# Kernel tuning notes

Measured on AMD Instinct MI355X. Metric: run time of the kernel, lower is better.

Reference implementation:

```python
import jax, jax.numpy as jnp
import numpy as np

LOG2 = float(np.log(2.0))

def shifted_softplus(x):
    return jax.nn.softplus(x) - LOG2

def setup_inputs() -> dict:
    key = jax.random.key(0)
    ks = jax.random.split(key, 12)
    N, E = 100000, 1600000
    Cin, Cout, F_, G = 128, 128, 128, 50
    x = jax.random.normal(ks[0], (N, Cin), dtype=jnp.float32)
    edge_index = jax.random.randint(ks[1], (2, E), 0, N, dtype=jnp.int64)
    edge_attr = jax.random.uniform(ks[2], (E, G), dtype=jnp.float32)
    s = lambda fan_in: 1.0 / np.sqrt(fan_in)
    lin1_w = jax.random.uniform(ks[3], (F_, Cin), jnp.float32, -s(Cin), s(Cin))
    lin1_b = jax.random.uniform(ks[4], (F_,), jnp.float32, -s(Cin), s(Cin))
    lin2_w = jax.random.uniform(ks[5], (Cout, F_), jnp.float32, -s(F_), s(F_))
    lin2_b = jax.random.uniform(ks[6], (Cout,), jnp.float32, -s(F_), s(F_))
    fn1_w = jax.random.uniform(ks[7], (F_, G), jnp.float32, -s(G), s(G))
    fn1_b = jax.random.uniform(ks[8], (F_,), jnp.float32, -s(G), s(G))
    fn2_w = jax.random.uniform(ks[9], (F_, F_), jnp.float32, -s(F_), s(F_))
    fn2_b = jax.random.uniform(ks[10], (F_,), jnp.float32, -s(F_), s(F_))
    return {"x": x, "edge_index": edge_index, "edge_attr": edge_attr,
            "lin1_w": lin1_w, "lin1_b": lin1_b, "lin2_w": lin2_w, "lin2_b": lin2_b,
            "fn1_w": fn1_w, "fn1_b": fn1_b, "fn2_w": fn2_w, "fn2_b": fn2_b}

def reference(x, edge_index, edge_attr, lin1_w, lin1_b, lin2_w, lin2_b,
              fn1_w, fn1_b, fn2_w, fn2_b):
    row, col = edge_index[0], edge_index[1]
    # filter network: [E, G] -> [E, F]
    W = shifted_softplus(edge_attr @ fn1_w.T + fn1_b) @ fn2_w.T + fn2_b
    # transform nodes then gather source features: [E, F]
    x_j = (x @ lin1_w.T + lin1_b)[col]
    msg = x_j * W
    # scatter-add over destination nodes: [N, F]
    agg = jax.ops.segment_sum(msg, row, num_segments=x.shape[0])
    return agg @ lin2_w.T + lin2_b
```

## Files before the change

### kernel.cpp

```cpp
#include <hip/hip_runtime.h>

#define NN 100000
#define NE 1600000
#define CC 128
#define GG 50
#define EPB 128
#define NSCB 98

typedef _Float16 half8 __attribute__((ext_vector_type(8)));
typedef _Float16 half2v __attribute__((ext_vector_type(2)));
typedef float f32x4 __attribute__((ext_vector_type(4)));

static __device__ __forceinline__ f32x4 mfma16(half8 a, half8 b, f32x4 c) {
    return __builtin_amdgcn_mfma_f32_16x16x32_f16(a, b, c, 0, 0, 0);
}

static __device__ __forceinline__ int perm_chan(int p) {
    return ((p >> 2) & 15) * 8 + (p >> 6) * 4 + (p & 3);
}

__global__ __launch_bounds__(256) void pack_frags(const float* fn1_w, const float* fn2_w,
                                                  _Float16* ws_frag)
{
    int tid = threadIdx.x;
    for (int s = tid; s < 1024; s += 256) {
        int l = s & 63, ks = (s >> 6) & 1, nb = s >> 7;
        int f = nb * 16 + (l & 15);
        int k0 = ks * 32 + 8 * (l >> 4);
        half8 v;
        #pragma unroll
        for (int i = 0; i < 8; i++) {
            int g = k0 + i;
            v[i] = (g < GG) ? (_Float16)fn1_w[f * GG + g] : (_Float16)0.f;
        }
        *reinterpret_cast<half8*>(&ws_frag[s * 8]) = v;
    }
    for (int s = tid; s < 2048; s += 256) {
        int l = s & 63, ks = (s >> 6) & 3, nb = s >> 8;
        int f = (l & 15) * 8 + nb;
        int k0 = ks * 32 + 8 * (l >> 4);
        const float* wp = fn2_w + f * CC + k0;
        half8 v;
        #pragma unroll
        for (int i = 0; i < 8; i++) v[i] = (_Float16)wp[i];
        *reinterpret_cast<half8*>(&ws_frag[8192 + s * 8]) = v;
    }
}

template <typename InT, typename OutT, bool DOH, bool PERMK>
__global__ __launch_bounds__(256) void lin_kernel(const InT* in, const float* w,
                                                  const float* bias, OutT* out, int nrows,
                                                  const int* hrow, int* hcnt)
{
    __shared__ __align__(16) _Float16 a_lds[64][136];
    __shared__ __align__(16) _Float16 bfrag[2048 * 8];

    int tid = threadIdx.x;
    int rowBase = blockIdx.x * 64;

    if constexpr (sizeof(InT) == 4) {
        for (int i = tid; i < 64 * 32; i += 256) {
            int r = i >> 5, c4 = i & 31;
            float4 v = {0.f, 0.f, 0.f, 0.f};
            if (rowBase + r < nrows)
                v = reinterpret_cast<const float4*>(in)[(size_t)(rowBase + r) * (CC / 4) + c4];
            a_lds[r][c4 * 4 + 0] = (_Float16)v.x;
            a_lds[r][c4 * 4 + 1] = (_Float16)v.y;
            a_lds[r][c4 * 4 + 2] = (_Float16)v.z;
            a_lds[r][c4 * 4 + 3] = (_Float16)v.w;
        }
    } else {
        for (int i = tid; i < 64 * 16; i += 256) {
            int r = i >> 4, c8 = i & 15;
            half8 v;
            #pragma unroll
            for (int k = 0; k < 8; k++) v[k] = (_Float16)0.f;
            if (rowBase + r < nrows)
                v = reinterpret_cast<const half8*>(in)[(size_t)(rowBase + r) * (CC / 8) + c8];
            *reinterpret_cast<half8*>(&a_lds[r][c8 * 8]) = v;
        }
    }
    for (int s = tid; s < 2048; s += 256) {
        int l = s & 63, ks = (s >> 6) & 3, nb = s >> 8;
        int f = nb * 16 + (l & 15);
        int k0 = ks * 32 + 8 * (l >> 4);
        const float* wrow = w + f * CC;
        half8 v;
        #pragma unroll
        for (int i = 0; i < 8; i++) {
            int k = k0 + i;
            int rk = PERMK ? perm_chan(k) : k;
            v[i] = (_Float16)wrow[rk];
        }
        *reinterpret_cast<half8*>(&bfrag[s * 8]) = v;
    }

    if constexpr (DOH) {
        int idx4 = blockIdx.x * 256 + tid;
        if (idx4 < NE / 4) {
            int4 e4 = reinterpret_cast<const int4*>(hrow)[idx4];
            atomicAdd(&hcnt[e4.x], 1);
            atomicAdd(&hcnt[e4.y], 1);
            atomicAdd(&hcnt[e4.z], 1);
            atomicAdd(&hcnt[e4.w], 1);
        }
    }
    __syncthreads();

    int wid = tid >> 6, l = tid & 63;
    int lr = l & 15, lg = l >> 4;
    int wrow = wid * 16;

    half8 afr[4];
    #pragma unroll
    for (int ks = 0; ks < 4; ks++)
        afr[ks] = *reinterpret_cast<const half8*>(&a_lds[wrow + lr][ks * 32 + 8 * lg]);

    #pragma unroll
    for (int nb = 0; nb < 8; nb++) {
        f32x4 acc = {0.f, 0.f, 0.f, 0.f};
        #pragma unroll
        for (int ks = 0; ks < 4; ks++) {
            half8 bf = *reinterpret_cast<const half8*>(&bfrag[((nb * 4 + ks) * 64 + l) * 8]);
            acc = mfma16(afr[ks], bf, acc);
        }
        float bv = bias[nb * 16 + lr];
        #pragma unroll
        for (int j = 0; j < 4; j++) {
            int r = rowBase + wrow + lg * 4 + j;
            if (r < nrows) out[(size_t)r * CC + nb * 16 + lr] = (OutT)(acc[j] + bv);
        }
    }
}

__global__ __launch_bounds__(256) void scanA(const int* cnt, int* excl, int* bsum, int n) {
    __shared__ int lds[256];
    int b = blockIdx.x, t = threadIdx.x;
    int base = b * 1024 + t * 4;
    int v[4];
    #pragma unroll
    for (int i = 0; i < 4; i++) v[i] = (base + i < n) ? cnt[base + i] : 0;
    int s = v[0] + v[1] + v[2] + v[3];
    lds[t] = s;
    __syncthreads();
    for (int off = 1; off < 256; off <<= 1) {
        int x = (t >= off) ? lds[t - off] : 0;
        __syncthreads();
        lds[t] += x;
        __syncthreads();
    }
    int incl = lds[t];
    int run = incl - s;
    #pragma unroll
    for (int i = 0; i < 4; i++) {
        if (base + i < n) excl[base + i] = run;
        run += v[i];
    }
    if (t == 255) bsum[b] = incl;
}

__global__ __launch_bounds__(128) void scanB(int* bsum, int n) {
    __shared__ int lds[128];
    int t = threadIdx.x;
    int v = (t < n) ? bsum[t] : 0;
    lds[t] = v;
    __syncthreads();
    for (int off = 1; off < 128; off <<= 1) {
        int x = (t >= off) ? lds[t - off] : 0;
        __syncthreads();
        lds[t] += x;
        __syncthreads();
    }
    if (t < n) bsum[t] = lds[t] - v;
}

__global__ __launch_bounds__(256) void scanC(int* excl, const int* bsum, int* cursor, int n) {
    int b = blockIdx.x, t = threadIdx.x;
    int off = bsum[b];
    int base = b * 1024 + t * 4;
    #pragma unroll
    for (int i = 0; i < 4; i++) {
        int idx = base + i;
        if (idx < n) {
            int val = excl[idx] + off;
            excl[idx] = val;
            cursor[idx] = val;
        }
    }
}

__global__ __launch_bounds__(512, 8) void msg_scatter_kernel(
    const _Float16* __restrict__ x1, const int* __restrict__ eidx,
    const float* __restrict__ ea, const _Float16* __restrict__ frag_ws,
    const float* __restrict__ fn1_b, const float* __restrict__ fn2_b,
    int* __restrict__ cursor, _Float16* __restrict__ msg)
{
    __shared__ __align__(16) unsigned char u_lds[EPB * CC * 2];
    __shared__ int cols_l[EPB];
    __shared__ int p_l[EPB];

    int tid = threadIdx.x;
    size_t eBase = (size_t)blockIdx.x * EPB;

    if (tid < EPB) {
        int r = eidx[eBase + tid];
        cols_l[tid] = eidx[(size_t)NE + eBase + tid];
        p_l[tid] = atomicAdd(&cursor[r], 1);
    }
    {
        const float2* eap = reinterpret_cast<const float2*>(ea + eBase * GG);
        for (int i = tid; i < EPB * 25; i += 512) {
            int e = i / 25, g2 = i - e * 25;
            float2 v = eap[i];
            int byte = e * 128 + ((g2 * 4) ^ ((e & 7) << 4));
            _Float16* p = reinterpret_cast<_Float16*>(u_lds + byte);
            p[0] = (_Float16)v.x;
            p[1] = (_Float16)v.y;
        }
        for (int i = tid; i < EPB * 14; i += 512) {
            int e = i / 14, g = (i - e * 14) + 50;
            int byte = e * 128 + ((g * 2) ^ ((e & 7) << 4));
            *reinterpret_cast<_Float16*>(u_lds + byte) = (_Float16)0.f;
        }
    }
    __syncthreads();

    int wv = tid >> 6, l = tid & 63;
    int lr = l & 15, lg = l >> 4;
    int erow = wv * 16;

    half8 a1[2];
    #pragma unroll
    for (int ks = 0; ks < 2; ks++) {
        int e = erow + lr;
        int byte = e * 128 + ((ks * 64 + lg * 16) ^ ((e & 7) << 4));
        a1[ks] = *reinterpret_cast<const half8*>(u_lds + byte);
    }
    __syncthreads();

    #pragma unroll
    for (int nb = 0; nb < 8; nb++) {
        half8 b10 = *reinterpret_cast<const half8*>(&frag_ws[((nb * 2 + 0) * 64 + l) * 8]);
        half8 b11 = *reinterpret_cast<const half8*>(&frag_ws[((nb * 2 + 1) * 64 + l) * 8]);
        f32x4 acc = {0.f, 0.f, 0.f, 0.f};
        acc = mfma16(a1[0], b10, acc);
        acc = mfma16(a1[1], b11, acc);
        float bv = fn1_b[nb * 16 + lr];
        int f = nb * 16 + lr;
        #pragma unroll
        for (int j = 0; j < 4; j++) {
            float z = acc[j] + bv;
            float t = __expf(-fabsf(z));
            float hz = fmaxf(z, 0.f) + __logf(1.f + t) - 0.69314718055994531f;
            int e = erow + lg * 4 + j;
            int byte = e * 256 + ((f * 2) ^ ((e & 7) << 4));
            *reinterpret_cast<_Float16*>(u_lds + byte) = (_Float16)hz;
        }
    }
    __syncthreads();

    half8 a2[4];
    #pragma unroll
    for (int ks = 0; ks < 4; ks++) {
        int e = erow + lr;
        int byte = e * 256 + ((ks * 64 + lg * 16) ^ ((e & 7) << 4));
        a2[ks] = *reinterpret_cast<const half8*>(u_lds + byte);
    }
    int pp[4], cc4[4];
    #pragma unroll
    for (int j = 0; j < 4; j++) {
        int e = erow + lg * 4 + j;
        pp[j] = p_l[e];
        cc4[j] = cols_l[e];
    }

    const half8* b2g = reinterpret_cast<const half8*>(frag_ws + 8192);
    #pragma unroll
    for (int hf = 0; hf < 2; hf++) {
        f32x4 acc[4];
        #pragma unroll
        for (int q = 0; q < 4; q++) {
            int nb = hf * 4 + q;
            f32x4 a = {0.f, 0.f, 0.f, 0.f};
            #pragma unroll
            for (int ks = 0; ks < 4; ks++)
                a = mfma16(a2[ks], b2g[(nb * 4 + ks) * 64 + l], a);
            acc[q] = a;
        }
        int ch0 = lr * 8 + hf * 4;
        int pos0 = hf * 64 + lr * 4;
        float4 bv = *reinterpret_cast<const float4*>(&fn2_b[ch0]);

        #pragma unroll
        for (int j = 0; j < 4; j++) {
            uint2 xp = *reinterpret_cast<const uint2*>(&x1[(size_t)cc4[j] * CC + ch0]);
            half2v x01 = __builtin_bit_cast(half2v, xp.x);
            half2v x23 = __builtin_bit_cast(half2v, xp.y);
            half2v p0, p1;
            p0[0] = (_Float16)((float)x01[0] * (acc[0][j] + bv.x));
            p0[1] = (_Float16)((float)x01[1] * (acc[1][j] + bv.y));
            p1[0] = (_Float16)((float)x23[0] * (acc[2][j] + bv.z));
            p1[1] = (_Float16)((float)x23[1] * (acc[3][j] + bv.w));
            uint2 st;
            st.x = __builtin_bit_cast(unsigned, p0);
            st.y = __builtin_bit_cast(unsigned, p1);
            *reinterpret_cast<uint2*>(&msg[(size_t)pp[j] * CC + pos0]) = st;
        }
    }
}

__global__ __launch_bounds__(512, 8) void gather_reduce_kernel(
    const _Float16* __restrict__ msg, const int* __restrict__ rowptr,
    _Float16* __restrict__ aggH)
{
    int tid = threadIdx.x;
    int r = blockIdx.x * 8 + (tid >> 6);
    int l = tid & 63;
    int e0 = rowptr[r];
    int e1 = (r == NN - 1) ? NE : rowptr[r + 1];

    const unsigned* base = reinterpret_cast<const unsigned*>(msg) + l;
    float a0 = 0.f, a1 = 0.f;
    int i = e0;
    for (; i + 1 < e1; i += 2) {
        unsigned v0 = base[(size_t)i * 64];
        unsigned v1 = base[(size_t)(i + 1) * 64];
        half2v h0 = __builtin_bit_cast(half2v, v0);
        half2v h1 = __builtin_bit_cast(half2v, v1);
        a0 += (float)h0[0] + (float)h1[0];
        a1 += (float)h0[1] + (float)h1[1];
    }
    if (i < e1) {
        half2v h = __builtin_bit_cast(half2v, base[(size_t)i * 64]);
        a0 += (float)h[0];
        a1 += (float)h[1];
    }
    half2v o;
    o[0] = (_Float16)a0;
    o[1] = (_Float16)a1;
    reinterpret_cast<unsigned*>(aggH)[(size_t)r * 64 + l] = __builtin_bit_cast(unsigned, o);
}

__global__ __launch_bounds__(512, 8) void edge_kernel_atomic(
    const _Float16* __restrict__ x1, const int* __restrict__ eidx,
    const float* __restrict__ ea, const _Float16* __restrict__ frag_ws,
    const float* __restrict__ fn1_b, const float* __restrict__ fn2_b,
    float* __restrict__ agg)
{
    __shared__ __align__(16) unsigned char u_lds[EPB * CC * 2];
    __shared__ int rows_l[EPB];
    __shared__ int cols_l[EPB];

    int tid = threadIdx.x;
    size_t eBase = (size_t)blockIdx.x * EPB;

    if (tid < EPB) {
        rows_l[tid] = eidx[eBase + tid];
        cols_l[tid] = eidx[(size_t)NE + eBase + tid];
    }
    {
        const float2* eap = reinterpret_cast<const float2*>(ea + eBase * GG);
        for (int i = tid; i < EPB * 25; i += 512) {
            int e = i / 25, g2 = i - e * 25;
            float2 v = eap[i];
            int byte = e * 128 + ((g2 * 4) ^ ((e & 7) << 4));
            _Float16* p = reinterpret_cast<_Float16*>(u_lds + byte);
            p[0] = (_Float16)v.x;
            p[1] = (_Float16)v.y;
        }
        for (int i = tid; i < EPB * 14; i += 512) {
            int e = i / 14, g = (i - e * 14) + 50;
            int byte = e * 128 + ((g * 2) ^ ((e & 7) << 4));
            *reinterpret_cast<_Float16*>(u_lds + byte) = (_Float16)0.f;
        }
    }
    __syncthreads();

    int wv = tid >> 6, l = tid & 63;
    int lr = l & 15, lg = l >> 4;
    int erow = wv * 16;

    half8 a1[2];
    #pragma unroll
    for (int ks = 0; ks < 2; ks++) {
        int e = erow + lr;
        int byte = e * 128 + ((ks * 64 + lg * 16) ^ ((e & 7) << 4));
        a1[ks] = *reinterpret_cast<const half8*>(u_lds + byte);
    }
    __syncthreads();

    #pragma unroll
    for (int nb = 0; nb < 8; nb++) {
        half8 b10 = *reinterpret_cast<const half8*>(&frag_ws[((nb * 2 + 0) * 64 + l) * 8]);
        half8 b11 = *reinterpret_cast<const half8*>(&frag_ws[((nb * 2 + 1) * 64 + l) * 8]);
        f32x4 acc = {0.f, 0.f, 0.f, 0.f};
        acc = mfma16(a1[0], b10, acc);
        acc = mfma16(a1[1], b11, acc);
        float bv = fn1_b[nb * 16 + lr];
        int f = nb * 16 + lr;
        #pragma unroll
        for (int j = 0; j < 4; j++) {
            float z = acc[j] + bv;
            float t = __expf(-fabsf(z));
            float hz = fmaxf(z, 0.f) + __logf(1.f + t) - 0.69314718055994531f;
            int e = erow + lg * 4 + j;
            int byte = e * 256 + ((f * 2) ^ ((e & 7) << 4));
            *reinterpret_cast<_Float16*>(u_lds + byte) = (_Float16)hz;
        }
    }
    __syncthreads();

    half8 a2[4];
    #pragma unroll
    for (int ks = 0; ks < 4; ks++) {
        int e = erow + lr;
        int byte = e * 256 + ((ks * 64 + lg * 16) ^ ((e & 7) << 4));
        a2[ks] = *reinterpret_cast<const half8*>(u_lds + byte);
    }
    int rr[4], cc4[4];
    #pragma unroll
    for (int j = 0; j < 4; j++) {
        int e = erow + lg * 4 + j;
        rr[j] = rows_l[e];
        cc4[j] = cols_l[e];
    }
    const half8* b2g = reinterpret_cast<const half8*>(frag_ws + 8192);
    #pragma unroll
    for (int hf = 0; hf < 2; hf++) {
        f32x4 acc[4];
        #pragma unroll
        for (int q = 0; q < 4; q++) {
            int nb = hf * 4 + q;
            f32x4 a = {0.f, 0.f, 0.f, 0.f};
            #pragma unroll
            for (int ks = 0; ks < 4; ks++)
                a = mfma16(a2[ks], b2g[(nb * 4 + ks) * 64 + l], a);
            acc[q] = a;
        }
        int ch0 = lr * 8 + hf * 4;
        float4 bv = *reinterpret_cast<const float4*>(&fn2_b[ch0]);
        #pragma unroll
        for (int j = 0; j < 4; j++) {
            uint2 xp = *reinterpret_cast<const uint2*>(&x1[(size_t)cc4[j] * CC + ch0]);
            half2v x01 = __builtin_bit_cast(half2v, xp.x);
            half2v x23 = __builtin_bit_cast(half2v, xp.y);
            float* dst = &agg[(size_t)rr[j] * CC + ch0];
            atomicAdd(dst + 0, (float)x01[0] * (acc[0][j] + bv.x));
            atomicAdd(dst + 1, (float)x01[1] * (acc[1][j] + bv.y));
            atomicAdd(dst + 2, (float)x23[0] * (acc[2][j] + bv.z));
            atomicAdd(dst + 3, (float)x23[1] * (acc[3][j] + bv.w));
        }
    }
}

extern "C" void kernel_launch(void* const* d_in, const int* in_sizes, int n_in,
                              void* d_out, int out_size, void* d_ws, size_t ws_size,
                              hipStream_t stream) {
    const float* x      = (const float*)d_in[0];
    const int*   eidx   = (const int*)d_in[1];
    const float* ea     = (const float*)d_in[2];
    const float* lin1_w = (const float*)d_in[3];
    const float* lin1_b = (const float*)d_in[4];
    const float* lin2_w = (const float*)d_in[5];
    const float* lin2_b = (const float*)d_in[6];
    const float* fn1_w  = (const float*)d_in[7];
    const float* fn1_b  = (const float*)d_in[8];
    const float* fn2_w  = (const float*)d_in[9];
    const float* fn2_b  = (const float*)d_in[10];

    float* out = (float*)d_out;

    const size_t o_frag = 0;
    const size_t o_x1h  = 65536;
    const size_t o_msg  = o_x1h + (size_t)NN * CC * 2;
    const size_t o_aggH = o_msg + (size_t)NE * CC * 2;
    const size_t o_cnt  = o_aggH + (size_t)NN * CC * 2;
    const size_t o_rp   = o_cnt + (size_t)NN * 4;
    const size_t o_cur  = o_rp + (size_t)NN * 4;
    const size_t o_bsum = o_cur + (size_t)NN * 4;
    const size_t req    = o_bsum + 512;

    _Float16* frag_ws = (_Float16*)((char*)d_ws + o_frag);
    _Float16* x1h     = (_Float16*)((char*)d_ws + o_x1h);

    pack_frags<<<1, 256, 0, stream>>>(fn1_w, fn2_w, frag_ws);

    if (ws_size >= req) {
        _Float16* msg  = (_Float16*)((char*)d_ws + o_msg);
        _Float16* aggH = (_Float16*)((char*)d_ws + o_aggH);
        int* cnt    = (int*)((char*)d_ws + o_cnt);
        int* rowptr = (int*)((char*)d_ws + o_rp);
        int* cursor = (int*)((char*)d_ws + o_cur);
        int* bsum   = (int*)((char*)d_ws + o_bsum);

        hipMemsetAsync(cnt, 0, (size_t)NN * 4, stream);
        lin_kernel<float, _Float16, true, false><<<(NN + 63) / 64, 256, 0, stream>>>(
            x, lin1_w, lin1_b, x1h, NN, eidx, cnt);
        scanA<<<NSCB, 256, 0, stream>>>(cnt, rowptr, bsum, NN);
        scanB<<<1, 128, 0, stream>>>(bsum, NSCB);
        scanC<<<NSCB, 256, 0, stream>>>(rowptr, bsum, cursor, NN);

        msg_scatter_kernel<<<NE / EPB, 512, 0, stream>>>(x1h, eidx, ea, frag_ws,
                                                         fn1_b, fn2_b, cursor, msg);
        gather_reduce_kernel<<<NN / 8, 512, 0, stream>>>(msg, rowptr, aggH);
        lin_kernel<_Float16, float, false, true><<<(NN + 63) / 64, 256, 0, stream>>>(
            aggH, lin2_w, lin2_b, out, NN, nullptr, nullptr);
    } else {
        lin_kernel<float, _Float16, false, false><<<(NN + 63) / 64, 256, 0, stream>>>(
            x, lin1_w, lin1_b, x1h, NN, nullptr, nullptr);
        hipMemsetAsync(out, 0, (size_t)NN * CC * sizeof(float), stream);
        edge_kernel_atomic<<<NE / EPB, 512, 0, stream>>>(x1h, eidx, ea, frag_ws,
                                                         fn1_b, fn2_b, out);
        lin_kernel<float, float, false, false><<<(NN + 63) / 64, 256, 0, stream>>>(
            out, lin2_w, lin2_b, out, NN, nullptr, nullptr);
    }
}
```

Baseline: 663.3 us.

## Write messages in edge order and gather via permutation index in reduce

```diff
diff --git a/kernel.cpp b/kernel.cpp
--- a/kernel.cpp
+++ b/kernel.cpp
@@ -193,11 +193,10 @@
     const _Float16* __restrict__ x1, const int* __restrict__ eidx,
     const float* __restrict__ ea, const _Float16* __restrict__ frag_ws,
     const float* __restrict__ fn1_b, const float* __restrict__ fn2_b,
-    int* __restrict__ cursor, _Float16* __restrict__ msg)
+    int* __restrict__ cursor, int* __restrict__ perm, _Float16* __restrict__ msg)
 {
     __shared__ __align__(16) unsigned char u_lds[EPB * CC * 2];
     __shared__ int cols_l[EPB];
-    __shared__ int p_l[EPB];
 
     int tid = threadIdx.x;
     size_t eBase = (size_t)blockIdx.x * EPB;
@@ -205,7 +204,8 @@
     if (tid < EPB) {
         int r = eidx[eBase + tid];
         cols_l[tid] = eidx[(size_t)NE + eBase + tid];
-        p_l[tid] = atomicAdd(&cursor[r], 1);
+        int p = atomicAdd(&cursor[r], 1);
+        perm[p] = (int)(eBase + tid);
     }
     {
         const float2* eap = reinterpret_cast<const float2*>(ea + eBase * GG);
@@ -266,13 +266,9 @@
         int byte = e * 256 + ((ks * 64 + lg * 16) ^ ((e & 7) << 4));
         a2[ks] = *reinterpret_cast<const half8*>(u_lds + byte);
     }
-    int pp[4], cc4[4];
-    #pragma unroll
-    for (int j = 0; j < 4; j++) {
-        int e = erow + lg * 4 + j;
-        pp[j] = p_l[e];
-        cc4[j] = cols_l[e];
-    }
+    int cc4[4];
+    #pragma unroll
+    for (int j = 0; j < 4; j++) cc4[j] = cols_l[erow + lg * 4 + j];
 
     const half8* b2g = reinterpret_cast<const half8*>(frag_ws + 8192);
     #pragma unroll
@@ -304,14 +300,15 @@
             uint2 st;
             st.x = __builtin_bit_cast(unsigned, p0);
             st.y = __builtin_bit_cast(unsigned, p1);
-            *reinterpret_cast<uint2*>(&msg[(size_t)pp[j] * CC + pos0]) = st;
+            size_t e = eBase + (size_t)(erow + lg * 4 + j);
+            *reinterpret_cast<uint2*>(&msg[e * CC + pos0]) = st;
         }
     }
 }
 
 __global__ __launch_bounds__(512, 8) void gather_reduce_kernel(
     const _Float16* __restrict__ msg, const int* __restrict__ rowptr,
-    _Float16* __restrict__ aggH)
+    const int* __restrict__ perm, _Float16* __restrict__ aggH)
 {
     int tid = threadIdx.x;
     int r = blockIdx.x * 8 + (tid >> 6);
@@ -319,19 +316,25 @@
     int e0 = rowptr[r];
     int e1 = (r == NN - 1) ? NE : rowptr[r + 1];
 
-    const unsigned* base = reinterpret_cast<const unsigned*>(msg) + l;
+    const unsigned* mb = reinterpret_cast<const unsigned*>(msg) + l;
     float a0 = 0.f, a1 = 0.f;
     int i = e0;
-    for (; i + 1 < e1; i += 2) {
-        unsigned v0 = base[(size_t)i * 64];
-        unsigned v1 = base[(size_t)(i + 1) * 64];
+    for (; i + 3 < e1; i += 4) {
+        int p0 = perm[i], p1 = perm[i + 1], p2 = perm[i + 2], p3 = perm[i + 3];
+        unsigned v0 = mb[(size_t)p0 * 64];
+        unsigned v1 = mb[(size_t)p1 * 64];
+        unsigned v2 = mb[(size_t)p2 * 64];
+        unsigned v3 = mb[(size_t)p3 * 64];
         half2v h0 = __builtin_bit_cast(half2v, v0);
         half2v h1 = __builtin_bit_cast(half2v, v1);
-        a0 += (float)h0[0] + (float)h1[0];
-        a1 += (float)h0[1] + (float)h1[1];
-    }
-    if (i < e1) {
-        half2v h = __builtin_bit_cast(half2v, base[(size_t)i * 64]);
+        half2v h2 = __builtin_bit_cast(half2v, v2);
+        half2v h3 = __builtin_bit_cast(half2v, v3);
+        a0 += ((float)h0[0] + (float)h1[0]) + ((float)h2[0] + (float)h3[0]);
+        a1 += ((float)h0[1] + (float)h1[1]) + ((float)h2[1] + (float)h3[1]);
+    }
+    for (; i < e1; i++) {
+        int p = perm[i];
+        half2v h = __builtin_bit_cast(half2v, mb[(size_t)p * 64]);
         a0 += (float)h[0];
         a1 += (float)h[1];
     }
@@ -478,7 +481,8 @@
     const size_t o_rp   = o_cnt + (size_t)NN * 4;
     const size_t o_cur  = o_rp + (size_t)NN * 4;
     const size_t o_bsum = o_cur + (size_t)NN * 4;
-    const size_t req    = o_bsum + 512;
+    const size_t o_perm = o_bsum + 512;
+    const size_t req    = o_perm + (size_t)NE * 4;
 
     _Float16* frag_ws = (_Float16*)((char*)d_ws + o_frag);
     _Float16* x1h     = (_Float16*)((char*)d_ws + o_x1h);
@@ -492,6 +496,7 @@
         int* rowptr = (int*)((char*)d_ws + o_rp);
         int* cursor = (int*)((char*)d_ws + o_cur);
         int* bsum   = (int*)((char*)d_ws + o_bsum);
+        int* perm   = (int*)((char*)d_ws + o_perm);
 
         hipMemsetAsync(cnt, 0, (size_t)NN * 4, stream);
         lin_kernel<float, _Float16, true, false><<<(NN + 63) / 64, 256, 0, stream>>>(
@@ -501,8 +506,8 @@
         scanC<<<NSCB, 256, 0, stream>>>(rowptr, bsum, cursor, NN);
 
         msg_scatter_kernel<<<NE / EPB, 512, 0, stream>>>(x1h, eidx, ea, frag_ws,
-                                                         fn1_b, fn2_b, cursor, msg);
-        gather_reduce_kernel<<<NN / 8, 512, 0, stream>>>(msg, rowptr, aggH);
+                                                         fn1_b, fn2_b, cursor, perm, msg);
+        gather_reduce_kernel<<<NN / 8, 512, 0, stream>>>(msg, rowptr, perm, aggH);
         lin_kernel<_Float16, float, false, true><<<(NN + 63) / 64, 256, 0, stream>>>(
             aggH, lin2_w, lin2_b, out, NN, nullptr, nullptr);
     } else {
```

After: 828.4 us. +24.9%, slower.
